# Performance work log

Hardware: AMD Instinct MI355X
Metric: run time of the kernel (lower is better)

## Reference

```python
import jax, jax.numpy as jnp
import numpy as np

N_NODES = 150018  # n_users + n_items + n_genres
LATENT_DIM = 64
N_LAYERS = 3
N_EDGES = 4_800_000


def setup_inputs() -> dict:
    key = jax.random.key(0)
    k1, k2, k3, k4 = jax.random.split(key, 4)
    embedding = jax.random.normal(k1, (N_NODES, LATENT_DIM), dtype=jnp.float32) * 0.01
    vals = jax.random.uniform(k2, (N_EDGES,), dtype=jnp.float32)
    rows = jax.random.randint(k3, (N_EDGES,), 0, N_NODES, dtype=jnp.int32)
    cols = jax.random.randint(k4, (N_EDGES,), 0, N_NODES, dtype=jnp.int32)
    return {"embedding": embedding, "vals": vals, "rows": rows, "cols": cols}


def _spmm(vals, rows, cols, x):
    # sparse.mm(adj, x): out[r] += vals[e] * x[cols[e]] for each edge e
    gathered = x[cols] * vals[:, None]  # [E, D]
    return jax.ops.segment_sum(gathered, rows, num_segments=N_NODES)


def reference(embedding, vals, rows, cols):
    # LightGCN-style propagation; dropout is identity in eval mode (training=False)
    emb = embedding
    acc = emb
    for _ in range(N_LAYERS):
        emb = _spmm(vals, rows, cols, emb)
        acc = acc + emb
    # mean over (n_layers + 1) stacked layer outputs
    return acc / jnp.asarray(N_LAYERS + 1, dtype=embedding.dtype)
```

## Files before the change

### kernel.cpp

```cpp
#include <hip/hip_runtime.h>

#define N_NODES 150018
#define DIMS 64
#define NELEM (N_NODES * DIMS)
#define NVEC4 (NELEM / 4)
#define NBKT ((N_NODES + 255) >> 8)
#define PADCAP 1792
#define SC_BLOCKS 512
#define SC_THREADS 1024
#define VINV 6.10388817e-05f

__device__ __forceinline__ unsigned short f2bf(float f) {
    unsigned int u = __float_as_uint(f);
    u += 0x7FFFu + ((u >> 16) & 1u);
    return (unsigned short)(u >> 16);
}
__device__ __forceinline__ float bf2f(unsigned short h) {
    return __uint_as_float(((unsigned int)h) << 16);
}

__global__ void conv_bf16_k(const float4* __restrict__ src, ushort4* __restrict__ dst, int n4) {
    int i = blockIdx.x * blockDim.x + threadIdx.x;
    if (i < n4) {
        float4 v = src[i];
        dst[i] = make_ushort4(f2bf(v.x), f2bf(v.y), f2bf(v.z), f2bf(v.w));
    }
}

__global__ __launch_bounds__(SC_THREADS) void hist_bucket_k(const int* __restrict__ rows,
                              int* __restrict__ counts, int n, int chunk) {
    __shared__ int h[NBKT];
    for (int i = threadIdx.x; i < NBKT; i += blockDim.x) h[i] = 0;
    __syncthreads();
    int beg = blockIdx.x * chunk;
    int end = min(n, beg + chunk);
    for (int e = beg + threadIdx.x; e < end; e += blockDim.x)
        atomicAdd(&h[rows[e] >> 8], 1);
    __syncthreads();
    for (int i = threadIdx.x; i < NBKT; i += blockDim.x)
        if (h[i]) atomicAdd(&counts[i], h[i]);
}

__global__ void scan_bucket_k(const int* __restrict__ counts, int* __restrict__ offs,
                              int* __restrict__ cursor, int n_edges) {
    __shared__ int s[1024];
    __shared__ int carry;
    if (threadIdx.x == 0) carry = 0;
    __syncthreads();
    for (int t = 0; t < NBKT; t += 1024) {
        int i = t + threadIdx.x;
        int v = (i < NBKT) ? counts[i] : 0;
        s[threadIdx.x] = v;
        __syncthreads();
        for (int off = 1; off < 1024; off <<= 1) {
            int tv = (threadIdx.x >= off) ? s[threadIdx.x - off] : 0;
            __syncthreads();
            s[threadIdx.x] += tv;
            __syncthreads();
        }
        if (i < NBKT) {
            int ex = carry + s[threadIdx.x] - v;
            offs[i] = ex;
            cursor[i] = ex;
        }
        __syncthreads();
        if (threadIdx.x == 1023) carry += s[1023];
        __syncthreads();
    }
    if (threadIdx.x == 0) offs[NBKT] = n_edges;
}

__global__ __launch_bounds__(SC_THREADS) void scatter_bucket_k(const int* __restrict__ rows,
                                 const int* __restrict__ cols,
                                 const float* __restrict__ vals, int* __restrict__ cursor,
                                 int2* __restrict__ edges1, int n, int chunk) {
    __shared__ int cnt[NBKT];
    __shared__ int base[NBKT];
    for (int i = threadIdx.x; i < NBKT; i += blockDim.x) cnt[i] = 0;
    __syncthreads();
    int beg = blockIdx.x * chunk;
    int end = min(n, beg + chunk);
    for (int e = beg + threadIdx.x; e < end; e += blockDim.x)
        atomicAdd(&cnt[rows[e] >> 8], 1);
    __syncthreads();
    for (int i = threadIdx.x; i < NBKT; i += blockDim.x) {
        int c = cnt[i];
        base[i] = c ? atomicAdd(&cursor[i], c) : 0;
        cnt[i] = 0;
    }
    __syncthreads();
    for (int e = beg + threadIdx.x; e < end; e += blockDim.x) {
        int r = rows[e];
        int b = r >> 8;
        int pos = base[b] + atomicAdd(&cnt[b], 1);
        edges1[pos] = make_int2(cols[e] | ((r & 255) << 18), __float_as_int(vals[e]));
    }
}

__global__ __launch_bounds__(512) void sort_bucket_k(const int2* __restrict__ e1,
                                 const int* __restrict__ bkt_offs,
                                 unsigned int* __restrict__ e2,
                                 int* __restrict__ row_offs) {
    __shared__ int cnt[256];
    __shared__ int pref[256];
    __shared__ int rank[256];
    int b = blockIdx.x;
    int beg = bkt_offs[b], end = bkt_offs[b + 1];
    int padbase = beg + b * PADCAP;
    if (threadIdx.x < 256) cnt[threadIdx.x] = 0;
    __syncthreads();
    for (int e = beg + threadIdx.x; e < end; e += 512)
        atomicAdd(&cnt[e1[e].x >> 18], 1);
    __syncthreads();
    int pc = 0;
    if (threadIdx.x < 256) {
        pc = (cnt[threadIdx.x] + 7) & ~7;
        pref[threadIdx.x] = pc;
    }
    __syncthreads();
    for (int off = 1; off < 256; off <<= 1) {
        int t = (threadIdx.x >= off && threadIdx.x < 256) ? pref[threadIdx.x - off] : 0;
        __syncthreads();
        if (threadIdx.x < 256) pref[threadIdx.x] += t;
        __syncthreads();
    }
    if (threadIdx.x < 256) {
        int ex = pref[threadIdx.x] - pc;
        row_offs[b * 257 + threadIdx.x] = padbase + ex;
        if (threadIdx.x == 255) row_offs[b * 257 + 256] = padbase + pref[255];
        pref[threadIdx.x] = ex;
        rank[threadIdx.x] = 0;
        int fb = padbase + ex + cnt[threadIdx.x];
        int fe = padbase + ex + pc;
        for (int i = fb; i < fe; ++i) e2[i] = 0u;
    }
    __syncthreads();
    for (int e = beg + threadIdx.x; e < end; e += 512) {
        int2 ed = e1[e];
        int slot = ed.x >> 18;
        float v = __int_as_float(ed.y);
        unsigned int q = (unsigned int)(v * 16383.0f + 0.5f);
        int pos = padbase + pref[slot] + atomicAdd(&rank[slot], 1);
        e2[pos] = (unsigned int)(ed.x & 0x3FFFF) | (q << 18);
    }
}

__global__ __launch_bounds__(256) void spmm_mid_k(const ushort4* __restrict__ xb,
                          const unsigned int* __restrict__ edges,
                          const int* __restrict__ row_offs,
                          ushort4* __restrict__ buf_out, int n_rows) {
    int row = (blockIdx.x * blockDim.x + threadIdx.x) >> 6;
    if (row >= n_rows) return;
    int lane = threadIdx.x & 63;
    int g = lane >> 4, q = lane & 15;
    int oi = (row >> 8) * 257 + (row & 255);
    int beg = row_offs[oi], end = row_offs[oi + 1];
    float4 a0 = make_float4(0.f, 0.f, 0.f, 0.f);
    float4 a1 = make_float4(0.f, 0.f, 0.f, 0.f);
    for (int e = beg; e < end; e += 8) {
        unsigned int w0 = edges[e + g];
        unsigned int w1 = edges[e + g + 4];
        ushort4 x0 = xb[((w0 & 0x3FFFFu) << 4) + q];
        ushort4 x1 = xb[((w1 & 0x3FFFFu) << 4) + q];
        float v0 = (float)(w0 >> 18) * VINV;
        float v1 = (float)(w1 >> 18) * VINV;
        a0.x = fmaf(v0, bf2f(x0.x), a0.x);  a0.y = fmaf(v0, bf2f(x0.y), a0.y);
        a0.z = fmaf(v0, bf2f(x0.z), a0.z);  a0.w = fmaf(v0, bf2f(x0.w), a0.w);
        a1.x = fmaf(v1, bf2f(x1.x), a1.x);  a1.y = fmaf(v1, bf2f(x1.y), a1.y);
        a1.w = fmaf(v1, bf2f(x1.w), a1.w);  a1.z = fmaf(v1, bf2f(x1.z), a1.z);
    }
    float4 a = make_float4(a0.x + a1.x, a0.y + a1.y, a0.z + a1.z, a0.w + a1.w);
    #pragma unroll
    for (int m = 16; m <= 32; m <<= 1) {
        a.x += __shfl_xor(a.x, m, 64);
        a.y += __shfl_xor(a.y, m, 64);
        a.z += __shfl_xor(a.z, m, 64);
        a.w += __shfl_xor(a.w, m, 64);
    }
    if (g == 0)
        buf_out[(row << 4) + q] = make_ushort4(f2bf(a.x), f2bf(a.y), f2bf(a.z), f2bf(a.w));
}

__global__ __launch_bounds__(256) void spmm_final_k(const ushort4* __restrict__ xb,
                          const unsigned int* __restrict__ edges,
                          const int* __restrict__ row_offs,
                          const ushort4* __restrict__ embb,
                          const ushort4* __restrict__ bufA,
                          const ushort4* __restrict__ bufB,
                          float4* __restrict__ out, int n_rows) {
    int row = (blockIdx.x * blockDim.x + threadIdx.x) >> 6;
    if (row >= n_rows) return;
    int lane = threadIdx.x & 63;
    int g = lane >> 4, q = lane & 15;
    int o = (row << 4) + q;

    ushort4 em = make_ushort4(0, 0, 0, 0);
    ushort4 ra = make_ushort4(0, 0, 0, 0), rb = make_ushort4(0, 0, 0, 0);
    if (g == 1) { em = embb[o]; ra = bufA[o]; rb = bufB[o]; }

    int oi = (row >> 8) * 257 + (row & 255);
    int beg = row_offs[oi], end = row_offs[oi + 1];
    float4 a0 = make_float4(0.f, 0.f, 0.f, 0.f);
    float4 a1 = make_float4(0.f, 0.f, 0.f, 0.f);
    for (int e = beg; e < end; e += 8) {
        unsigned int w0 = edges[e + g];
        unsigned int w1 = edges[e + g + 4];
        ushort4 x0 = xb[((w0 & 0x3FFFFu) << 4) + q];
        ushort4 x1 = xb[((w1 & 0x3FFFFu) << 4) + q];
        float v0 = (float)(w0 >> 18) * VINV;
        float v1 = (float)(w1 >> 18) * VINV;
        a0.x = fmaf(v0, bf2f(x0.x), a0.x);  a0.y = fmaf(v0, bf2f(x0.y), a0.y);
        a0.z = fmaf(v0, bf2f(x0.z), a0.z);  a0.w = fmaf(v0, bf2f(x0.w), a0.w);
        a1.x = fmaf(v1, bf2f(x1.x), a1.x);  a1.y = fmaf(v1, bf2f(x1.y), a1.y);
        a1.z = fmaf(v1, bf2f(x1.z), a1.z);  a1.w = fmaf(v1, bf2f(x1.w), a1.w);
    }
    float4 a = make_float4(a0.x + a1.x, a0.y + a1.y, a0.z + a1.z, a0.w + a1.w);
    #pragma unroll
    for (int m = 16; m <= 32; m <<= 1) {
        a.x += __shfl_xor(a.x, m, 64);
        a.y += __shfl_xor(a.y, m, 64);
        a.z += __shfl_xor(a.z, m, 64);
        a.w += __shfl_xor(a.w, m, 64);
    }
    if (g == 1) {
        float4 r;
        r.x = (bf2f(em.x) + bf2f(ra.x) + bf2f(rb.x) + a.x) * 0.25f;
        r.y = (bf2f(em.y) + bf2f(ra.y) + bf2f(rb.y) + a.y) * 0.25f;
        r.z = (bf2f(em.z) + bf2f(ra.z) + bf2f(rb.z) + a.z) * 0.25f;
        r.w = (bf2f(em.w) + bf2f(ra.w) + bf2f(rb.w) + a.w) * 0.25f;
        out[o] = r;
    }
}

extern "C" void kernel_launch(void* const* d_in, const int* in_sizes, int n_in,
                              void* d_out, int out_size, void* d_ws, size_t ws_size,
                              hipStream_t stream) {
    const float* emb  = (const float*)d_in[0];
    const float* vals = (const float*)d_in[1];
    const int*   rows = (const int*)d_in[2];
    const int*   cols = (const int*)d_in[3];
    float*       out  = (float*)d_out;
    const int n_edges = in_sizes[1];

    char* w = (char*)d_ws;
    int2*   edges1 = (int2*)w;
    ushort* bufAb  = (ushort*)w;
    ushort* bufBb  = (ushort*)(w + (size_t)NELEM * 2);
    w += (size_t)NELEM * 4;
    unsigned int* edges2 = (unsigned int*)w;
    w += ((size_t)n_edges + (size_t)NBKT * PADCAP) * 4;
    ushort* embb   = (ushort*)w; w += (size_t)NELEM * 2;
    int* counts    = (int*)w;    w += (size_t)NBKT * 4;
    int* bkt_offs  = (int*)w;    w += (size_t)(NBKT + 1) * 4;
    int* cursor    = (int*)w;    w += (size_t)NBKT * 4;
    int* row_offs  = (int*)w;

    const int chunk = (n_edges + SC_BLOCKS - 1) / SC_BLOCKS;

    hipMemsetAsync(counts, 0, (size_t)NBKT * 4, stream);
    hist_bucket_k<<<SC_BLOCKS, SC_THREADS, 0, stream>>>(rows, counts, n_edges, chunk);
    scan_bucket_k<<<1, 1024, 0, stream>>>(counts, bkt_offs, cursor, n_edges);
    scatter_bucket_k<<<SC_BLOCKS, SC_THREADS, 0, stream>>>(rows, cols, vals, cursor,
                                                           edges1, n_edges, chunk);
    sort_bucket_k<<<NBKT, 512, 0, stream>>>(edges1, bkt_offs, edges2, row_offs);
    conv_bf16_k<<<(NVEC4 + 255) / 256, 256, 0, stream>>>((const float4*)emb,
                                                         (ushort4*)embb, NVEC4);

    const int sp_grid = (N_NODES + 3) / 4;
    spmm_mid_k<<<sp_grid, 256, 0, stream>>>((const ushort4*)embb, edges2, row_offs,
                                            (ushort4*)bufAb, N_NODES);
    spmm_mid_k<<<sp_grid, 256, 0, stream>>>((const ushort4*)bufAb, edges2, row_offs,
                                            (ushort4*)bufBb, N_NODES);
    spmm_final_k<<<sp_grid, 256, 0, stream>>>((const ushort4*)bufBb, edges2, row_offs,
                                              (const ushort4*)embb, (const ushort4*)bufAb,
                                              (const ushort4*)bufBb, (float4*)out, N_NODES);
}
```

Baseline: 418.5 us.

## Stage bucket scatter in shared memory for coalesced bucketed writes

```diff
diff --git a/kernel.cpp b/kernel.cpp
--- a/kernel.cpp
+++ b/kernel.cpp
@@ -6,8 +6,9 @@
 #define NVEC4 (NELEM / 4)
 #define NBKT ((N_NODES + 255) >> 8)
 #define PADCAP 1792
-#define SC_BLOCKS 512
-#define SC_THREADS 1024
+#define HIST_BLOCKS 512
+#define CH 8192
+#define EPP 8
 #define VINV 6.10388817e-05f
 
 __device__ __forceinline__ unsigned short f2bf(float f) {
@@ -27,7 +28,7 @@
     }
 }
 
-__global__ __launch_bounds__(SC_THREADS) void hist_bucket_k(const int* __restrict__ rows,
+__global__ __launch_bounds__(1024) void hist_bucket_k(const int* __restrict__ rows,
                               int* __restrict__ counts, int n, int chunk) {
     __shared__ int h[NBKT];
     for (int i = threadIdx.x; i < NBKT; i += blockDim.x) h[i] = 0;
@@ -70,30 +71,68 @@
     if (threadIdx.x == 0) offs[NBKT] = n_edges;
 }
 
-__global__ __launch_bounds__(SC_THREADS) void scatter_bucket_k(const int* __restrict__ rows,
+__global__ __launch_bounds__(1024) void scatter_bucket_k(const int* __restrict__ rows,
                                  const int* __restrict__ cols,
                                  const float* __restrict__ vals, int* __restrict__ cursor,
-                                 int2* __restrict__ edges1, int n, int chunk) {
+                                 int2* __restrict__ edges1, int n) {
+    __shared__ int2 staged[CH];
     __shared__ int cnt[NBKT];
     __shared__ int base[NBKT];
-    for (int i = threadIdx.x; i < NBKT; i += blockDim.x) cnt[i] = 0;
-    __syncthreads();
-    int beg = blockIdx.x * chunk;
-    int end = min(n, beg + chunk);
-    for (int e = beg + threadIdx.x; e < end; e += blockDim.x)
-        atomicAdd(&cnt[rows[e] >> 8], 1);
-    __syncthreads();
-    for (int i = threadIdx.x; i < NBKT; i += blockDim.x) {
+    __shared__ int lofs[NBKT];
+    __shared__ int s[1024];
+    const int t = threadIdx.x;
+    const int beg = blockIdx.x * CH;
+    const int end = min(n, beg + CH);
+    const int cn = end - beg;
+
+    for (int i = t; i < NBKT; i += 1024) cnt[i] = 0;
+    __syncthreads();
+
+    int er[EPP], ec[EPP];
+    float ev[EPP];
+    #pragma unroll
+    for (int k = 0; k < EPP; ++k) {
+        int e = beg + t + (k << 10);
+        if (e < end) {
+            er[k] = rows[e]; ec[k] = cols[e]; ev[k] = vals[e];
+            atomicAdd(&cnt[er[k] >> 8], 1);
+        } else er[k] = -1;
+    }
+    __syncthreads();
+
+    for (int i = t; i < NBKT; i += 1024) {
         int c = cnt[i];
         base[i] = c ? atomicAdd(&cursor[i], c) : 0;
-        cnt[i] = 0;
-    }
-    __syncthreads();
-    for (int e = beg + threadIdx.x; e < end; e += blockDim.x) {
-        int r = rows[e];
-        int b = r >> 8;
-        int pos = base[b] + atomicAdd(&cnt[b], 1);
-        edges1[pos] = make_int2(cols[e] | ((r & 255) << 18), __float_as_int(vals[e]));
+    }
+    int v = (t < NBKT) ? cnt[t] : 0;
+    s[t] = v;
+    __syncthreads();
+    for (int off = 1; off < 1024; off <<= 1) {
+        int tv = (t >= off) ? s[t - off] : 0;
+        __syncthreads();
+        s[t] += tv;
+        __syncthreads();
+    }
+    if (t < NBKT) { lofs[t] = s[t] - v; cnt[t] = 0; }
+    __syncthreads();
+
+    #pragma unroll
+    for (int k = 0; k < EPP; ++k) {
+        if (er[k] >= 0) {
+            int b = er[k] >> 8;
+            int p = lofs[b] + atomicAdd(&cnt[b], 1);
+            unsigned int q = (unsigned int)(ev[k] * 16383.0f + 0.5f);
+            staged[p] = make_int2(ec[k] | ((er[k] & 255) << 18),
+                                  (int)(q | ((unsigned int)b << 14)));
+        }
+    }
+    __syncthreads();
+
+    for (int i = t; i < cn; i += 1024) {
+        int2 st = staged[i];
+        int b = ((unsigned int)st.y) >> 14;
+        int gpos = base[b] + i - lofs[b];
+        edges1[gpos] = make_int2(st.x, st.y & 0x3FFF);
     }
 }
 
@@ -138,10 +177,8 @@
     for (int e = beg + threadIdx.x; e < end; e += 512) {
         int2 ed = e1[e];
         int slot = ed.x >> 18;
-        float v = __int_as_float(ed.y);
-        unsigned int q = (unsigned int)(v * 16383.0f + 0.5f);
         int pos = padbase + pref[slot] + atomicAdd(&rank[slot], 1);
-        e2[pos] = (unsigned int)(ed.x & 0x3FFFF) | (q << 18);
+        e2[pos] = (unsigned int)(ed.x & 0x3FFFF) | (((unsigned int)ed.y) << 18);
     }
 }
 
@@ -167,7 +204,7 @@
         a0.x = fmaf(v0, bf2f(x0.x), a0.x);  a0.y = fmaf(v0, bf2f(x0.y), a0.y);
         a0.z = fmaf(v0, bf2f(x0.z), a0.z);  a0.w = fmaf(v0, bf2f(x0.w), a0.w);
         a1.x = fmaf(v1, bf2f(x1.x), a1.x);  a1.y = fmaf(v1, bf2f(x1.y), a1.y);
-        a1.w = fmaf(v1, bf2f(x1.w), a1.w);  a1.z = fmaf(v1, bf2f(x1.z), a1.z);
+        a1.z = fmaf(v1, bf2f(x1.z), a1.z);  a1.w = fmaf(v1, bf2f(x1.w), a1.w);
     }
     float4 a = make_float4(a0.x + a1.x, a0.y + a1.y, a0.z + a1.z, a0.w + a1.w);
     #pragma unroll
@@ -255,13 +292,13 @@
     int* cursor    = (int*)w;    w += (size_t)NBKT * 4;
     int* row_offs  = (int*)w;
 
-    const int chunk = (n_edges + SC_BLOCKS - 1) / SC_BLOCKS;
+    const int hchunk = (n_edges + HIST_BLOCKS - 1) / HIST_BLOCKS;
+    const int scb = (n_edges + CH - 1) / CH;
 
     hipMemsetAsync(counts, 0, (size_t)NBKT * 4, stream);
-    hist_bucket_k<<<SC_BLOCKS, SC_THREADS, 0, stream>>>(rows, counts, n_edges, chunk);
+    hist_bucket_k<<<HIST_BLOCKS, 1024, 0, stream>>>(rows, counts, n_edges, hchunk);
     scan_bucket_k<<<1, 1024, 0, stream>>>(counts, bkt_offs, cursor, n_edges);
-    scatter_bucket_k<<<SC_BLOCKS, SC_THREADS, 0, stream>>>(rows, cols, vals, cursor,
-                                                           edges1, n_edges, chunk);
+    scatter_bucket_k<<<scb, 1024, 0, stream>>>(rows, cols, vals, cursor, edges1, n_edges);
     sort_bucket_k<<<NBKT, 512, 0, stream>>>(edges1, bkt_offs, edges2, row_offs);
     conv_bf16_k<<<(NVEC4 + 255) / 256, 256, 0, stream>>>((const float4*)emb,
                                                          (ushort4*)embb, NVEC4);
```

Result: faster. 394.2 us (-5.8%).
